# Optimization experiments

Measured on AMD Instinct MI355X. Metric: run time of the kernel, lower is better.

## Reference

```python
import jax, jax.numpy as jnp
import numpy as np

N_TAU = 100  # steps per delay: dt = tau / N_TAU (backward code uses dt = 0.01*tau)


def F_model(x, y, t, W1, W2, b):
    # F(x(t), x(t - tau), t); t enters the signature but this Model is autonomous,
    # matching the repo's example models.
    return jnp.tanh(W1 @ x + W2 @ y + b)


def setup_inputs() -> dict:
    key = jax.random.key(0)
    d = 512
    k1, k2, k3, k4 = jax.random.split(key, 4)
    scale = 1.0 / np.sqrt(d).astype(np.float32)
    x_0 = jax.random.normal(k1, (d,), dtype=jnp.float32)
    W1 = jax.random.normal(k2, (d, d), dtype=jnp.float32) * scale
    W2 = jax.random.normal(k3, (d, d), dtype=jnp.float32) * scale
    b = jax.random.normal(k4, (d,), dtype=jnp.float32)
    tau = jnp.ones((), dtype=jnp.float32)  # time delay; dt = 0.01 * tau
    N = 2000  # = floor(T / dt) with T = 20, tau = 1
    return {"x_0": x_0, "tau": tau, "W1": W1, "W2": W2, "b": b, "N": N}


def reference(x_0, tau, W1, W2, b, N):
    """Forward-Euler DDE solve of x'(t) = F(x(t), x(t - tau), t), x(t) = x_0 for t <= 0.
    Returns the trajectory as a [d, N+1] array (kth column = state at step k),
    matching DDE_Solver's x_Trajectory layout."""
    d = x_0.shape[0]
    M = N_TAU + 1  # ring buffer holds the last N_tau+1 states
    dt = 0.01 * tau

    buf0 = jnp.zeros((d, M), dtype=x_0.dtype).at[:, 0].set(x_0)

    def step(buf, j):
        x_j = buf[:, j % M]
        # delayed state x(t_j - tau) = x_{j - N_tau}; (j - N_tau) % M == (j + 1) % M
        y_hist = buf[:, (j + 1) % M]
        y_j = jnp.where(j >= N_TAU, y_hist, x_0)  # pre-history: x(t) = x_0
        t_j = j * dt
        x_jp1 = x_j + dt * F_model(x_j, y_j, t_j, W1, W2, b)
        buf = buf.at[:, (j + 1) % M].set(x_jp1)
        return buf, x_jp1

    _, ys = jax.lax.scan(step, buf0, jnp.arange(N))  # ys: [N, d]
    return jnp.concatenate([x_0[:, None], ys.T], axis=1)  # [d, N+1]
```

## Files before the change

### kernel.cpp

```cpp
#include <hip/hip_runtime.h>


#define D    512
#define NTAU 100
#define M    112
#define QD   101
#define NW   64

typedef unsigned long long u64;

__device__ __forceinline__ float lo_f(u64 v){ union{unsigned u; float f;} c; c.u=(unsigned)v; return c.f; }
__device__ __forceinline__ u64 pack_rec(unsigned tag, float x){ union{unsigned u; float f;} c; c.f=x; return ((u64)tag<<32)|(u64)c.u; }
__device__ __forceinline__ u64 ag_ld(const u64* p){
    return __hip_atomic_load(p, __ATOMIC_RELAXED, __HIP_MEMORY_SCOPE_AGENT);
}
__device__ __forceinline__ void ag_st(u64* p, u64 v){
    __hip_atomic_store(p, v, __ATOMIC_RELAXED, __HIP_MEMORY_SCOPE_AGENT);
}
__device__ __forceinline__ void iss8(const u64* p, u64 r[8]){
    #pragma unroll
    for (int i = 0; i < 8; ++i) r[i] = ag_ld(p + 64 * i);
}
__device__ __forceinline__ bool chk8m(const u64 r[8], unsigned t, int i0, bool ownm){
    bool ok = true;
    #pragma unroll
    for (int i = 0; i < 8; ++i)
        ok &= (((unsigned)(r[i] >> 32) == t) || (ownm && i == i0));
    return __all(ok);
}
__device__ __forceinline__ float sel8(const float* a, int k){
    float s = a[0];
    s = (k == 1) ? a[1] : s;  s = (k == 2) ? a[2] : s;
    s = (k == 3) ? a[3] : s;  s = (k == 4) ? a[4] : s;
    s = (k == 5) ? a[5] : s;  s = (k == 6) ? a[6] : s;
    s = (k == 7) ? a[7] : s;
    return s;
}
__device__ __forceinline__ float reduce8(float a[8], int sel){
    #pragma unroll
    for (int r = 0; r < 8; ++r){
        a[r] += __shfl_xor(a[r], 1, 64);
        a[r] += __shfl_xor(a[r], 2, 64);
        a[r] += __shfl_xor(a[r], 4, 64);
    }
    float d = sel8(a, sel);
    d += __shfl_xor(d, 8, 64);
    d += __shfl_xor(d, 16, 64);
    d += __shfl_xor(d, 32, 64);
    return d;
}

__global__ __launch_bounds__(64)
__attribute__((amdgpu_waves_per_eu(1, 1)))
void ndde_r9(
    const float* __restrict__ x0p, const float* __restrict__ taup,
    const float* __restrict__ W1,  const float* __restrict__ W2,
    const float* __restrict__ bb,  const int* __restrict__ Np,
    float* __restrict__ out, u64* __restrict__ ring, float one)
{
    __shared__ float qlds[QD * 8];

    const int lane    = threadIdx.x & 63;
    const int wb      = blockIdx.x;
    const int rowbase = wb * 8;
    const int N       = Np[0];
    const float dt    = 0.01f * taup[0];
    const int sel     = lane & 7;
    const int i0      = wb >> 3;
    const int lb      = (wb * 8) & 63;
    const bool ownm   = ((unsigned)(lane - lb)) < 8u;

    float w1v[8][8], w2v[8][8];
    #pragma unroll
    for (int r = 0; r < 8; ++r){
        const float* p1 = W1 + (size_t)(rowbase + r) * D + lane;
        const float* p2 = W2 + (size_t)(rowbase + r) * D + lane;
        #pragma unroll
        for (int i = 0; i < 8; ++i){
            w1v[r][i] = p1[64 * i] * one;
            w2v[r][i] = p2[64 * i] * one;
        }
    }
    #pragma unroll
    for (int r = 0; r < 8; ++r){
        #pragma unroll
        for (int i = 0; i < 8; ++i)
            asm volatile("" : "+v"(w1v[r][i]), "+v"(w2v[r][i]));
    }

    float xv0[8];
    #pragma unroll
    for (int i = 0; i < 8; ++i) xv0[i] = x0p[64 * i + lane];
    float ax[8], ay[8];
    #pragma unroll
    for (int r = 0; r < 8; ++r){
        float st = 0.f, sy = 0.f;
        #pragma unroll
        for (int i = 0; i < 8; ++i){
            st = fmaf(w1v[r][i], xv0[i], st);
            sy = fmaf(w2v[r][i], xv0[i], sy);
        }
        ax[r] = st; ay[r] = sy;
    }
    const float xdot0 = reduce8(ax, sel);
    const float q0    = reduce8(ay, sel);
    if (lane < 8) qlds[0 * 8 + lane] = q0;

    float xloc = 0.f, bval = 0.f;
    if (lane < 8){
        const int row = rowbase + lane;
        xloc = x0p[row];
        bval = bb[row];
        out[(size_t)row * (N + 1)] = xloc;
        if (N >= 1){
            const float x1 = xloc + dt * tanhf(xdot0 + q0 + bval);
            xloc = x1;
            ag_st(ring + D + row, pack_rec(2u, x1));
            out[(size_t)row * (N + 1) + 1] = x1;
        }
    }

    u64 cur[8];
    iss8(ring + (size_t)1 * D + lane, cur);

    float obuf[16];
    #pragma unroll
    for (int k = 0; k < 16; ++k) obuf[k] = 0.f;

    int sx = 1, sp = 2;
    int qw = 1, qr = 0;
    bool dead = false;

    for (int j = 1; j < N && !dead; ++j){
        const unsigned tx = (unsigned)(j + 1);
        const u64* px = ring + (size_t)sx * D + lane;

        float ydot = 0.f;
        if (lane < 8) ydot = qlds[qr * 8 + lane];

        if (!chk8m(cur, tx, i0, ownm)){
            u64 alt[8];
            iss8(px, alt);
            int it = 0;
            for (;;){
                iss8(px, cur);
                if (chk8m(alt, tx, i0, ownm)){
                    #pragma unroll
                    for (int i = 0; i < 8; ++i) cur[i] = alt[i];
                    break;
                }
                iss8(px, alt);
                if (chk8m(cur, tx, i0, ownm)) break;
                if ((it += 2) > (1 << 21)){ dead = true; break; }
            }
        }
        float xf[8];
        #pragma unroll
        for (int i = 0; i < 8; ++i) xf[i] = lo_f(cur[i]);
        {
            const float xsub = __shfl(xloc, lane - lb, 64);
            #pragma unroll
            for (int i = 0; i < 8; ++i)
                xf[i] = (ownm && i == i0) ? xsub : xf[i];
        }

        float a[8];
        #pragma unroll
        for (int r = 0; r < 8; ++r){
            float s = 0.f;
            #pragma unroll
            for (int i = 0; i < 8; ++i) s = fmaf(w1v[r][i], xf[i], s);
            a[r] = s;
        }
        const float xdot = reduce8(a, sel);

        float xn = 0.f;
        if (lane < 8){
            xn = xloc + dt * tanhf(xdot + ydot + bval);
            xloc = xn;
        }

        iss8(ring + (size_t)sp * D + lane, cur);
        if (lane < 8)
            ag_st(ring + (size_t)sp * D + (rowbase + lane), pack_rec(tx + 1, xn));

        float c[8];
        #pragma unroll
        for (int r = 0; r < 8; ++r){
            float s = 0.f;
            #pragma unroll
            for (int i = 0; i < 8; ++i) s = fmaf(w2v[r][i], xf[i], s);
            c[r] = s;
        }
        const float qj = reduce8(c, sel);
        if (lane < 8) qlds[qw * 8 + lane] = qj;

        if (lane < 8){
            #pragma unroll
            for (int k = 0; k < 15; ++k) obuf[k] = obuf[k + 1];
            obuf[15] = xn;
            if (((j - 1) & 15) == 15){
                float* po = out + (size_t)(rowbase + lane) * (N + 1) + (j - 14);
                #pragma unroll
                for (int k = 0; k < 16; ++k) po[k] = obuf[k];
            }
        }

        sx = sp;
        sp = (sp == M - 1) ? 0 : sp + 1;
        qw = (qw == QD - 1) ? 0 : qw + 1;
        if (j >= NTAU) qr = (qr == QD - 1) ? 0 : qr + 1;
    }

    if (N >= 2 && lane < 8){
        const int cnt = ((N - 2) & 15) + 1;
        float* po = out + (size_t)(rowbase + lane) * (N + 1);
        #pragma unroll
        for (int k = 0; k < 16; ++k){
            if (k >= 16 - cnt) po[N - 15 + k] = obuf[k];
        }
    }
}

extern "C" void kernel_launch(void* const* d_in, const int* in_sizes, int n_in,
                              void* d_out, int out_size, void* d_ws, size_t ws_size,
                              hipStream_t stream)
{
    const float* x0  = (const float*)d_in[0];
    const float* tau = (const float*)d_in[1];
    const float* W1  = (const float*)d_in[2];
    const float* W2  = (const float*)d_in[3];
    const float* b   = (const float*)d_in[4];
    const int*   Np  = (const int*)  d_in[5];

    u64* ring = (u64*)d_ws;
    const float one = 1.0f;

    hipLaunchKernelGGL(ndde_r9, dim3(NW), dim3(64), 0, stream,
                       x0, tau, W1, W2, b, Np, (float*)d_out, ring, one);
}
```

Baseline: 3.314 ms.

## Poll per-block signal flags before reading tagged ring records

Each block now publishes one release-ordered flag per step in a separate signal array, and consumers first spin on a single 32-bit flag per lane before loading the eight tagged 64-bit ring records, instead of polling all records directly. The own-block local substitution and the speculative prefetch of the next slot are removed. The register-pinning asm, the multiply-by-one trick and the waves_per_eu attribute are also dropped. This adds an extra dependent round trip per step (flag, then data) in exchange for lighter polling traffic, and it may raise register pressure or latency on the critical serial path.

```diff
diff --git a/kernel.cpp b/kernel.cpp
--- a/kernel.cpp
+++ b/kernel.cpp
@@ -17,15 +17,17 @@
 __device__ __forceinline__ void ag_st(u64* p, u64 v){
     __hip_atomic_store(p, v, __ATOMIC_RELAXED, __HIP_MEMORY_SCOPE_AGENT);
 }
+__device__ __forceinline__ unsigned ag_ldu(const unsigned* p){
+    return __hip_atomic_load(p, __ATOMIC_RELAXED, __HIP_MEMORY_SCOPE_AGENT);
+}
 __device__ __forceinline__ void iss8(const u64* p, u64 r[8]){
     #pragma unroll
     for (int i = 0; i < 8; ++i) r[i] = ag_ld(p + 64 * i);
 }
-__device__ __forceinline__ bool chk8m(const u64 r[8], unsigned t, int i0, bool ownm){
+__device__ __forceinline__ bool chk8(const u64 r[8], unsigned t){
     bool ok = true;
     #pragma unroll
-    for (int i = 0; i < 8; ++i)
-        ok &= (((unsigned)(r[i] >> 32) == t) || (ownm && i == i0));
+    for (int i = 0; i < 8; ++i) ok &= ((unsigned)(r[i] >> 32) == t);
     return __all(ok);
 }
 __device__ __forceinline__ float sel8(const float* a, int k){
@@ -50,13 +52,12 @@
     return d;
 }
 
-__global__ __launch_bounds__(64)
-__attribute__((amdgpu_waves_per_eu(1, 1)))
-void ndde_r9(
+__global__ __launch_bounds__(64) void ndde_r10(
     const float* __restrict__ x0p, const float* __restrict__ taup,
     const float* __restrict__ W1,  const float* __restrict__ W2,
     const float* __restrict__ bb,  const int* __restrict__ Np,
-    float* __restrict__ out, u64* __restrict__ ring, float one)
+    float* __restrict__ out, u64* __restrict__ ring,
+    unsigned* __restrict__ sig)
 {
     __shared__ float qlds[QD * 8];
 
@@ -66,9 +67,6 @@
     const int N       = Np[0];
     const float dt    = 0.01f * taup[0];
     const int sel     = lane & 7;
-    const int i0      = wb >> 3;
-    const int lb      = (wb * 8) & 63;
-    const bool ownm   = ((unsigned)(lane - lb)) < 8u;
 
     float w1v[8][8], w2v[8][8];
     #pragma unroll
@@ -77,15 +75,9 @@
         const float* p2 = W2 + (size_t)(rowbase + r) * D + lane;
         #pragma unroll
         for (int i = 0; i < 8; ++i){
-            w1v[r][i] = p1[64 * i] * one;
-            w2v[r][i] = p2[64 * i] * one;
-        }
-    }
-    #pragma unroll
-    for (int r = 0; r < 8; ++r){
-        #pragma unroll
-        for (int i = 0; i < 8; ++i)
-            asm volatile("" : "+v"(w1v[r][i]), "+v"(w2v[r][i]));
+            w1v[r][i] = p1[64 * i];
+            w2v[r][i] = p2[64 * i];
+        }
     }
 
     float xv0[8];
@@ -119,9 +111,9 @@
             out[(size_t)row * (N + 1) + 1] = x1;
         }
     }
-
-    u64 cur[8];
-    iss8(ring + (size_t)1 * D + lane, cur);
+    if (N >= 1 && lane == 0)
+        __hip_atomic_store(&sig[1 * NW + wb], 2u,
+                           __ATOMIC_RELEASE, __HIP_MEMORY_SCOPE_AGENT);
 
     float obuf[16];
     #pragma unroll
@@ -133,36 +125,37 @@
 
     for (int j = 1; j < N && !dead; ++j){
         const unsigned tx = (unsigned)(j + 1);
-        const u64* px = ring + (size_t)sx * D + lane;
+        const unsigned* ps = sig + (size_t)sx * NW + lane;
 
         float ydot = 0.f;
         if (lane < 8) ydot = qlds[qr * 8 + lane];
 
-        if (!chk8m(cur, tx, i0, ownm)){
-            u64 alt[8];
-            iss8(px, alt);
+        unsigned sA = ag_ldu(ps);
+        if (!__all(sA == tx)){
+            unsigned sB = ag_ldu(ps);
             int it = 0;
             for (;;){
+                sA = ag_ldu(ps);
+                if (__all(sB == tx)) break;
+                sB = ag_ldu(ps);
+                if (__all(sA == tx)) break;
+                if ((it += 2) > (1 << 20)){ dead = true; break; }
+            }
+        }
+
+        u64 cur[8];
+        const u64* px = ring + (size_t)sx * D + lane;
+        iss8(px, cur);
+        if (!chk8(cur, tx)){
+            int it2 = 0;
+            do {
                 iss8(px, cur);
-                if (chk8m(alt, tx, i0, ownm)){
-                    #pragma unroll
-                    for (int i = 0; i < 8; ++i) cur[i] = alt[i];
-                    break;
-                }
-                iss8(px, alt);
-                if (chk8m(cur, tx, i0, ownm)) break;
-                if ((it += 2) > (1 << 21)){ dead = true; break; }
-            }
+                if (++it2 > (1 << 16)){ dead = true; break; }
+            } while (!chk8(cur, tx));
         }
         float xf[8];
         #pragma unroll
         for (int i = 0; i < 8; ++i) xf[i] = lo_f(cur[i]);
-        {
-            const float xsub = __shfl(xloc, lane - lb, 64);
-            #pragma unroll
-            for (int i = 0; i < 8; ++i)
-                xf[i] = (ownm && i == i0) ? xsub : xf[i];
-        }
 
         float a[8];
         #pragma unroll
@@ -178,11 +171,11 @@
         if (lane < 8){
             xn = xloc + dt * tanhf(xdot + ydot + bval);
             xloc = xn;
-        }
-
-        iss8(ring + (size_t)sp * D + lane, cur);
-        if (lane < 8)
             ag_st(ring + (size_t)sp * D + (rowbase + lane), pack_rec(tx + 1, xn));
+        }
+        if (lane == 0)
+            __hip_atomic_store(&sig[(size_t)sp * NW + wb], tx + 1,
+                               __ATOMIC_RELEASE, __HIP_MEMORY_SCOPE_AGENT);
 
         float c[8];
         #pragma unroll
@@ -233,9 +226,9 @@
     const float* b   = (const float*)d_in[4];
     const int*   Np  = (const int*)  d_in[5];
 
-    u64* ring = (u64*)d_ws;
-    const float one = 1.0f;
-
-    hipLaunchKernelGGL(ndde_r9, dim3(NW), dim3(64), 0, stream,
-                       x0, tau, W1, W2, b, Np, (float*)d_out, ring, one);
-}
+    u64*      ring = (u64*)d_ws;
+    unsigned* sig  = (unsigned*)((char*)d_ws + (size_t)M * D * 8);
+
+    hipLaunchKernelGGL(ndde_r10, dim3(NW), dim3(64), 0, stream,
+                       x0, tau, W1, W2, b, Np, (float*)d_out, ring, sig);
+}
```

Measured after the change: 5.445 ms. 64.3% more time.
